# Performance work log

Hardware: AMD Instinct MI355X
Metric: run time of the kernel (lower is better)

## Reference

```python
import jax, jax.numpy as jnp
import numpy as np

N_NODES = 100000
NEG_SLOPE = 0.2  # PyG GATConv default leaky_relu slope


def _gat_conv(x, src, dst, W, a_src, a_dst, b, heads, out_c, concat):
    """One PyG-style GATConv (eval mode, dropout disabled).
    x: [N, F_in]; src/dst: [E] (src -> dst message direction, self-loops included).
    """
    N = x.shape[0]
    h = (x @ W).reshape(N, heads, out_c)                      # [N, H, C]
    alpha_s = jnp.einsum('nhc,hc->nh', h, a_src)              # [N, H]
    alpha_d = jnp.einsum('nhc,hc->nh', h, a_dst)              # [N, H]
    e = jax.nn.leaky_relu(alpha_s[src] + alpha_d[dst], NEG_SLOPE)  # [E, H]
    # segment softmax over incoming edges of each destination node
    e_max = jax.ops.segment_max(e, dst, num_segments=N)       # [N, H]
    e_exp = jnp.exp(e - e_max[dst])                           # [E, H]
    denom = jax.ops.segment_sum(e_exp, dst, num_segments=N)   # [N, H]
    alpha = e_exp / (denom[dst] + 1e-16)                      # [E, H]
    msg = h[src] * alpha[:, :, None]                          # [E, H, C]
    out = jax.ops.segment_sum(msg, dst, num_segments=N)       # [N, H, C]
    out = out.reshape(N, heads * out_c) if concat else out.mean(axis=1)
    return out + b


def setup_inputs() -> dict:
    key = jax.random.key(0)
    ks = jax.random.split(key, 16)
    N, E, F_in = N_NODES, 400000, 128
    H = 4
    h1, h2, out_dim = 128, 64, 2

    def glorot(k, shape, fan_in):
        return jax.random.normal(k, shape, dtype=jnp.float32) * (1.0 / np.sqrt(fan_in))

    inp = {
        'x': jax.random.normal(ks[0], (N, F_in), dtype=jnp.float32),
        'edge_index': jax.random.randint(ks[1], (2, E), 0, N, dtype=jnp.int64),
        'W1': glorot(ks[2], (F_in, H * h1), F_in),
        'a_src1': glorot(ks[3], (H, h1), h1),
        'a_dst1': glorot(ks[4], (H, h1), h1),
        'b1': jnp.zeros((H * h1,), dtype=jnp.float32),
        'W2': glorot(ks[5], (H * h1, H * h2), H * h1),
        'a_src2': glorot(ks[6], (H, h2), h2),
        'a_dst2': glorot(ks[7], (H, h2), h2),
        'b2': jnp.zeros((H * h2,), dtype=jnp.float32),
        # layer 3: 256 -> 2, heads=1, concat=False (mean)
        'W3': glorot(ks[8], (H * h2, 1 * out_dim), H * h2),
        'a_src3': glorot(ks[9], (1, out_dim), out_dim),
        'a_dst3': glorot(ks[10], (1, out_dim), out_dim),
        'b3': jnp.zeros((out_dim,), dtype=jnp.float32),
    }
    return inp


def reference(x, edge_index, W1, a_src1, a_dst1, b1, W2, a_src2, a_dst2, b2,
              W3, a_src3, a_dst3, b3):
    N = x.shape[0]
    # add self-loops (PyG GATConv default add_self_loops=True)
    loop = jnp.arange(N, dtype=edge_index.dtype)
    src = jnp.concatenate([edge_index[0], loop])
    dst = jnp.concatenate([edge_index[1], loop])

    h = _gat_conv(x, src, dst, W1, a_src1, a_dst1, b1, heads=4, out_c=128, concat=True)
    h = jax.nn.elu(h)  # dropout is identity in eval mode
    h = _gat_conv(h, src, dst, W2, a_src2, a_dst2, b2, heads=4, out_c=64, concat=True)
    h = jax.nn.elu(h)
    out = _gat_conv(h, src, dst, W3, a_src3, a_dst3, b3, heads=1, out_c=2, concat=False)
    return out
```

## Files before the change

### kernel.cpp

```cpp
#include <hip/hip_runtime.h>
#include <hip/hip_bf16.h>
#include <math.h>


#define LEAKY_SLOPE 0.2f

typedef __attribute__((ext_vector_type(8))) short bf16x8;
typedef __attribute__((ext_vector_type(4))) float f32x4;
typedef __attribute__((ext_vector_type(4))) float fx4;

__device__ __forceinline__ unsigned short f2bf(float f) {
    unsigned int x = __float_as_uint(f);
    x += 0x7fffu + ((x >> 16) & 1u);
    return (unsigned short)(x >> 16);
}
__device__ __forceinline__ float bf2f(unsigned short u) {
    return __uint_as_float(((unsigned int)u) << 16);
}
__device__ __forceinline__ float elu(float x) {
    return (x > 0.f) ? x : (__expf(x) - 1.f);
}

__device__ __forceinline__ void gll16(const void* g, void* l) {
    __builtin_amdgcn_global_load_lds((const __attribute__((address_space(1))) void*)g,
                                     (__attribute__((address_space(3))) void*)l, 16, 0, 0);
}

__device__ __forceinline__ int edge_val(const int* __restrict__ ei, int is64, long long idx) {
    return is64 ? ei[2 * idx] : ei[idx];
}

__global__ void detect_kernel(const unsigned int* __restrict__ ei, int* __restrict__ flag) {
    int lane = threadIdx.x;
    unsigned int v = ei[2 * lane + 1];
    unsigned long long b = __ballot(v != 0u);
    if (lane == 0) *flag = (b == 0ull) ? 1 : 0;
}

__global__ __launch_bounds__(256) void zero2_kernel(int* __restrict__ a, int* __restrict__ b, int n) {
    int i = blockIdx.x * blockDim.x + threadIdx.x;
    if (i < n) { a[i] = 0; b[i] = 0; }
}

__global__ __launch_bounds__(256) void sentinel_kernel(float* __restrict__ out, int n, float v) {
    int i = blockIdx.x * blockDim.x + threadIdx.x;
    if (i < n) out[i] = v;
}

__global__ __launch_bounds__(256) void count_kernel(const int* __restrict__ ei,
                                                    const int* __restrict__ flag,
                                                    int E, int N, int* __restrict__ counts) {
    int e = blockIdx.x * blockDim.x + threadIdx.x;
    if (e >= E + N) return;
    int is64 = *flag;
    int d = (e < E) ? edge_val(ei, is64, (long long)E + e) : (e - E);
    atomicAdd(&counts[d], 1);
}

__global__ __launch_bounds__(256) void scan_block_kernel(const int* __restrict__ counts,
                                                         int* __restrict__ ptrArr,
                                                         int* __restrict__ bsums, int N) {
    __shared__ int sh[256];
    int t = threadIdx.x, i = blockIdx.x * 256 + t;
    int v = (i < N) ? counts[i] : 0;
    sh[t] = v;
    __syncthreads();
    for (int off = 1; off < 256; off <<= 1) {
        int u = (t >= off) ? sh[t - off] : 0;
        __syncthreads();
        sh[t] += u;
        __syncthreads();
    }
    if (i < N) ptrArr[i] = sh[t] - v;
    if (t == 255) bsums[blockIdx.x] = sh[255];
}

__global__ __launch_bounds__(1024) void scan_tops_kernel(const int* __restrict__ bsums,
                                                         int* __restrict__ boff, int nb,
                                                         int* __restrict__ totalOut) {
    __shared__ int sh[1024];
    int t = threadIdx.x;
    int v = (t < nb) ? bsums[t] : 0;
    sh[t] = v;
    __syncthreads();
    for (int off = 1; off < 1024; off <<= 1) {
        int u = (t >= off) ? sh[t - off] : 0;
        __syncthreads();
        sh[t] += u;
        __syncthreads();
    }
    if (t < nb) boff[t] = sh[t] - v;
    if (t == 1023) *totalOut = sh[1023];
}

__global__ __launch_bounds__(256) void scan_add_kernel(int* __restrict__ ptrArr,
                                                       const int* __restrict__ boff, int N) {
    int i = blockIdx.x * blockDim.x + threadIdx.x;
    if (i < N) ptrArr[i] += boff[i >> 8];
}

__global__ __launch_bounds__(256) void fill_kernel(const int* __restrict__ ei,
                                                   const int* __restrict__ flag,
                                                   int E, int N,
                                                   const int* __restrict__ ptrArr,
                                                   int* __restrict__ cursor,
                                                   int* __restrict__ csr_src) {
    int e = blockIdx.x * blockDim.x + threadIdx.x;
    if (e >= E + N) return;
    int is64 = *flag;
    int s, d;
    if (e < E) {
        s = edge_val(ei, is64, e);
        d = edge_val(ei, is64, (long long)E + e);
    } else {
        s = d = e - E;
    }
    int slot = atomicAdd(&cursor[d], 1);
    csr_src[ptrArr[d] + slot] = s;
}

__global__ __launch_bounds__(256) void transpose_w_kernel(const float* __restrict__ W,
                                                          unsigned short* __restrict__ Wt,
                                                          int K, int Nn) {
    int i = blockIdx.x * blockDim.x + threadIdx.x;
    if (i >= K * Nn) return;
    int n = i / K, k = i - n * K;
    Wt[i] = f2bf(W[(size_t)k * Nn + n]);
}

__global__ __launch_bounds__(256) void proj_attn_kernel(const float* __restrict__ W1,
                                                        const float* __restrict__ a_s,
                                                        const float* __restrict__ a_d,
                                                        float* __restrict__ ws1,
                                                        float* __restrict__ wd1) {
    int t = blockIdx.x * blockDim.x + threadIdx.x;
    if (t >= 1024) return;
    int k = t >> 3, sd = (t >> 2) & 1, h = t & 3;
    const float* a = sd ? a_d : a_s;
    float s = 0.f;
    const float* wr = W1 + (size_t)k * 512 + h * 128;
    const float* ar = a + h * 128;
    for (int c = 0; c < 128; ++c) s += wr[c] * ar[c];
    (sd ? wd1 : ws1)[k * 4 + h] = s;
}

__global__ __launch_bounds__(256) void alpha_x_kernel(const float* __restrict__ x,
                                                      const float* __restrict__ ws1,
                                                      const float* __restrict__ wd1,
                                                      float* __restrict__ out_s,
                                                      float* __restrict__ out_d,
                                                      unsigned short* __restrict__ xbf, int N) {
    int lane = threadIdx.x & 63;
    int wid = threadIdx.x >> 6;
    int n = blockIdx.x * (blockDim.x >> 6) + wid;
    if (n >= N) return;
    int k0 = lane * 2;
    float2 xv = *(const float2*)(x + (size_t)n * 128 + k0);
    alignas(4) unsigned short o[2] = {f2bf(xv.x), f2bf(xv.y)};
    *(unsigned int*)(xbf + (size_t)n * 128 + k0) = *(unsigned int*)o;
    fx4 s0 = *(const fx4*)(ws1 + k0 * 4);
    fx4 s1 = *(const fx4*)(ws1 + k0 * 4 + 4);
    fx4 d0 = *(const fx4*)(wd1 + k0 * 4);
    fx4 d1 = *(const fx4*)(wd1 + k0 * 4 + 4);
    float ps[4], pd[4];
#pragma unroll
    for (int h = 0; h < 4; ++h) {
        ps[h] = xv.x * s0[h] + xv.y * s1[h];
        pd[h] = xv.x * d0[h] + xv.y * d1[h];
    }
#pragma unroll
    for (int off = 32; off; off >>= 1)
#pragma unroll
        for (int h = 0; h < 4; ++h) {
            ps[h] += __shfl_xor(ps[h], off);
            pd[h] += __shfl_xor(pd[h], off);
        }
    if (lane == 0) {
        fx4 rs = {ps[0], ps[1], ps[2], ps[3]};
        fx4 rd = {pd[0], pd[1], pd[2], pd[3]};
        *(fx4*)(out_s + (size_t)n * 4) = rs;
        *(fx4*)(out_d + (size_t)n * 4) = rd;
    }
}

__global__ __launch_bounds__(256) void sm_aggx_kernel(const int* __restrict__ ptrArr,
                                                      const int* __restrict__ csr_src,
                                                      const float* __restrict__ as,
                                                      const float* __restrict__ ad,
                                                      const unsigned short* __restrict__ xbf,
                                                      unsigned short* __restrict__ aggX, int N) {
    __shared__ float sal[4][64][4];
    int lane = threadIdx.x & 63;
    int wid = threadIdx.x >> 6;
    int n = blockIdx.x * 4 + wid;
    if (n >= N) return;
    int beg = ptrArr[n], end = ptrArr[n + 1];
    int deg = end - beg;
    fx4 dv = *(const fx4*)(ad + (size_t)n * 4);
    float acc[4][2];
#pragma unroll
    for (int h = 0; h < 4; ++h) { acc[h][0] = 0.f; acc[h][1] = 0.f; }

    if (deg <= 64) {
        bool act = lane < deg;
        int i = beg + (act ? lane : 0);
        int s = csr_src[i];
        fx4 av = *(const fx4*)(as + (size_t)s * 4);
        float e[4];
#pragma unroll
        for (int h = 0; h < 4; ++h) {
            float xx = av[h] + dv[h];
            xx = (xx >= 0.f) ? xx : LEAKY_SLOPE * xx;
            e[h] = act ? xx : -INFINITY;
        }
#pragma unroll
        for (int h = 0; h < 4; ++h) {
            float mm = e[h];
#pragma unroll
            for (int off = 32; off; off >>= 1) mm = fmaxf(mm, __shfl_xor(mm, off));
            float ex = __expf(e[h] - mm);
            float ss = ex;
#pragma unroll
            for (int off = 32; off; off >>= 1) ss += __shfl_xor(ss, off);
            sal[wid][lane][h] = ex / (ss + 1e-16f);
        }
        for (int i2 = beg; i2 < end; i2 += 4) {
            int r = end - i2;
            int e1 = (r > 1) ? i2 + 1 : i2;
            int e2 = (r > 2) ? i2 + 2 : i2;
            int e3 = (r > 3) ? i2 + 3 : i2;
            int s0 = csr_src[i2], s1 = csr_src[e1], s2 = csr_src[e2], s3 = csr_src[e3];
            fx4 a0 = *(const fx4*)&sal[wid][i2 - beg][0];
            fx4 a1 = *(const fx4*)&sal[wid][e1 - beg][0];
            fx4 a2 = *(const fx4*)&sal[wid][e2 - beg][0];
            fx4 a3 = *(const fx4*)&sal[wid][e3 - beg][0];
            if (r <= 1) a1 = (fx4){0.f, 0.f, 0.f, 0.f};
            if (r <= 2) a2 = (fx4){0.f, 0.f, 0.f, 0.f};
            if (r <= 3) a3 = (fx4){0.f, 0.f, 0.f, 0.f};
            unsigned int r0 = *(const unsigned int*)(xbf + (size_t)s0 * 128 + lane * 2);
            unsigned int r1 = *(const unsigned int*)(xbf + (size_t)s1 * 128 + lane * 2);
            unsigned int r2 = *(const unsigned int*)(xbf + (size_t)s2 * 128 + lane * 2);
            unsigned int r3 = *(const unsigned int*)(xbf + (size_t)s3 * 128 + lane * 2);
            float x00 = bf2f((unsigned short)r0), x01 = bf2f((unsigned short)(r0 >> 16));
            float x10 = bf2f((unsigned short)r1), x11 = bf2f((unsigned short)(r1 >> 16));
            float x20 = bf2f((unsigned short)r2), x21 = bf2f((unsigned short)(r2 >> 16));
            float x30 = bf2f((unsigned short)r3), x31 = bf2f((unsigned short)(r3 >> 16));
#pragma unroll
            for (int h = 0; h < 4; ++h) {
                acc[h][0] += a0[h] * x00 + a1[h] * x10 + a2[h] * x20 + a3[h] * x30;
                acc[h][1] += a0[h] * x01 + a1[h] * x11 + a2[h] * x21 + a3[h] * x31;
            }
        }
    } else {
        float m[4], inv[4];
#pragma unroll
        for (int h = 0; h < 4; ++h) m[h] = -INFINITY;
        for (int i = beg + lane; i < end; i += 64) {
            int s = csr_src[i];
            fx4 av = *(const fx4*)(as + (size_t)s * 4);
#pragma unroll
            for (int h = 0; h < 4; ++h) {
                float v = av[h] + dv[h];
                v = (v >= 0.f) ? v : LEAKY_SLOPE * v;
                m[h] = fmaxf(m[h], v);
            }
        }
#pragma unroll
        for (int h = 0; h < 4; ++h)
#pragma unroll
            for (int off = 32; off; off >>= 1) m[h] = fmaxf(m[h], __shfl_xor(m[h], off));
        float ss[4] = {0.f, 0.f, 0.f, 0.f};
        for (int i = beg + lane; i < end; i += 64) {
            int s = csr_src[i];
            fx4 av = *(const fx4*)(as + (size_t)s * 4);
#pragma unroll
            for (int h = 0; h < 4; ++h) {
                float v = av[h] + dv[h];
                v = (v >= 0.f) ? v : LEAKY_SLOPE * v;
                ss[h] += __expf(v - m[h]);
            }
        }
#pragma unroll
        for (int h = 0; h < 4; ++h) {
#pragma unroll
            for (int off = 32; off; off >>= 1) ss[h] += __shfl_xor(ss[h], off);
            inv[h] = 1.f / (ss[h] + 1e-16f);
        }
        for (int i = beg; i < end; ++i) {
            int s = csr_src[i];
            fx4 av = *(const fx4*)(as + (size_t)s * 4);
            unsigned int rr = *(const unsigned int*)(xbf + (size_t)s * 128 + lane * 2);
            float x0 = bf2f((unsigned short)rr), x1 = bf2f((unsigned short)(rr >> 16));
#pragma unroll
            for (int h = 0; h < 4; ++h) {
                float v = av[h] + dv[h];
                v = (v >= 0.f) ? v : LEAKY_SLOPE * v;
                float al = __expf(v - m[h]) * inv[h];
                acc[h][0] += al * x0;
                acc[h][1] += al * x1;
            }
        }
    }
#pragma unroll
    for (int h = 0; h < 4; ++h) {
        alignas(4) unsigned short o[2] = {f2bf(acc[h][0]), f2bf(acc[h][1])};
        *(unsigned int*)(aggX + (size_t)h * N * 128 + (size_t)n * 128 + lane * 2) = *(unsigned int*)o;
    }
}

__global__ __launch_bounds__(256) void fused12_kernel(const unsigned short* __restrict__ aggX,
                                                      const unsigned short* __restrict__ Wt1,
                                                      const unsigned short* __restrict__ Wt2,
                                                      const float* __restrict__ b1,
                                                      const float* __restrict__ a_src2,
                                                      const float* __restrict__ a_dst2,
                                                      unsigned short* __restrict__ h2,
                                                      float* __restrict__ alpha_s,
                                                      float* __restrict__ alpha_d,
                                                      int M) {
    __shared__ unsigned short h1[64 * 512];
    __shared__ unsigned short stg[4 * 64 * 128];
    const int bm = blockIdx.x;
    const int tid = threadIdx.x;
    const int lane = tid & 63, wid = tid >> 6;
    const int l15 = lane & 15, l4 = lane >> 4;

    const unsigned short* plane = aggX + (size_t)wid * M * 128;
    {
        char* base = (char*)stg + wid * 16384;
#pragma unroll
        for (int it = 0; it < 16; ++it) {
            int idx = it * 64 + lane;
            int row = idx >> 4, ch = idx & 15;
            int src = ch ^ (row & 7);
            int grow = bm * 64 + row;
            if (grow < M) gll16(plane + (size_t)grow * 128 + src * 8, base + it * 1024);
        }
    }
    __syncthreads();

    const char* Asw = (const char*)stg + wid * 16384;
    f32x4 acc[4][4];

    for (int half = 0; half < 2; ++half) {
#pragma unroll
        for (int m = 0; m < 4; ++m)
#pragma unroll
            for (int n = 0; n < 4; ++n) acc[m][n] = (f32x4){0.f, 0.f, 0.f, 0.f};
#pragma unroll
        for (int step = 0; step < 4; ++step) {
            bf16x8 af[4], bfr[4];
            int kb = step * 64 + l4 * 16;
#pragma unroll
            for (int m = 0; m < 4; ++m) {
                int rl = m * 16 + l15;
                af[m] = *(const bf16x8*)(Asw + rl * 256 + (kb ^ ((rl & 7) << 4)));
            }
#pragma unroll
            for (int n = 0; n < 4; ++n) {
                int rB = wid * 128 + half * 64 + n * 16 + l15;
                bfr[n] = *(const bf16x8*)(Wt1 + (size_t)rB * 128 + step * 32 + l4 * 8);
            }
#pragma unroll
            for (int m = 0; m < 4; ++m)
#pragma unroll
                for (int n = 0; n < 4; ++n)
                    acc[m][n] = __builtin_amdgcn_mfma_f32_16x16x32_bf16(bfr[n], af[m], acc[m][n], 0, 0, 0);
        }
#pragma unroll
        for (int m = 0; m < 4; ++m) {
            int rl = m * 16 + l15;
#pragma unroll
            for (int n = 0; n < 4; ++n) {
                int col = wid * 128 + half * 64 + n * 16 + l4 * 4;
                fx4 bb = *(const fx4*)(b1 + col);
                f32x4 v = acc[m][n];
                alignas(8) unsigned short o[4];
#pragma unroll
                for (int j = 0; j < 4; ++j) o[j] = f2bf(elu(v[j] + bb[j]));
                int byteoff = (col * 2) ^ ((rl & 7) << 4);
                *(uint2*)((char*)h1 + rl * 1024 + byteoff) = *(uint2*)o;
            }
        }
    }
    __syncthreads();

#pragma unroll
    for (int m = 0; m < 4; ++m)
#pragma unroll
        for (int n = 0; n < 4; ++n) acc[m][n] = (f32x4){0.f, 0.f, 0.f, 0.f};
    for (int step = 0; step < 16; ++step) {
        bf16x8 af[4], bfr[4];
        int kb = step * 64 + l4 * 16;
#pragma unroll
        for (int m = 0; m < 4; ++m) {
            int rl = m * 16 + l15;
            af[m] = *(const bf16x8*)((const char*)h1 + rl * 1024 + (kb ^ ((rl & 7) << 4)));
        }
#pragma unroll
        for (int n = 0; n < 4; ++n) {
            int rB = wid * 64 + n * 16 + l15;
            bfr[n] = *(const bf16x8*)(Wt2 + (size_t)rB * 512 + step * 32 + l4 * 8);
        }
#pragma unroll
        for (int m = 0; m < 4; ++m)
#pragma unroll
            for (int n = 0; n < 4; ++n)
                acc[m][n] = __builtin_amdgcn_mfma_f32_16x16x32_bf16(bfr[n], af[m], acc[m][n], 0, 0, 0);
    }
#pragma unroll
    for (int m = 0; m < 4; ++m) {
        int row = bm * 64 + m * 16 + l15;
        if (row < M) {
#pragma unroll
            for (int n = 0; n < 4; ++n) {
                int col = wid * 64 + n * 16 + l4 * 4;
                f32x4 v = acc[m][n];
                alignas(8) unsigned short o[4] = {f2bf(v[0]), f2bf(v[1]), f2bf(v[2]), f2bf(v[3])};
                *(uint2*)(h2 + (size_t)row * 256 + col) = *(uint2*)o;
            }
        }
    }
    float ps[4], pd[4];
#pragma unroll
    for (int m = 0; m < 4; ++m) { ps[m] = 0.f; pd[m] = 0.f; }
#pragma unroll
    for (int n = 0; n < 4; ++n) {
        int col = wid * 64 + n * 16 + l4 * 4;
        fx4 asv = *(const fx4*)(a_src2 + col);
        fx4 adv = *(const fx4*)(a_dst2 + col);
#pragma unroll
        for (int m = 0; m < 4; ++m)
#pragma unroll
            for (int j = 0; j < 4; ++j) {
                ps[m] += acc[m][n][j] * asv[j];
                pd[m] += acc[m][n][j] * adv[j];
            }
    }
#pragma unroll
    for (int m = 0; m < 4; ++m) {
        ps[m] += __shfl_xor(ps[m], 16); ps[m] += __shfl_xor(ps[m], 32);
        pd[m] += __shfl_xor(pd[m], 16); pd[m] += __shfl_xor(pd[m], 32);
    }
    if (lane < 16) {
#pragma unroll
        for (int m = 0; m < 4; ++m) {
            int row = bm * 64 + m * 16 + l15;
            if (row < M) {
                alpha_s[(size_t)row * 4 + wid] = ps[m];
                alpha_d[(size_t)row * 4 + wid] = pd[m];
            }
        }
    }
}

__global__ __launch_bounds__(256) void sm_agg2_kernel(const int* __restrict__ ptrArr,
                                                      const int* __restrict__ csr_src,
                                                      const float* __restrict__ as,
                                                      const float* __restrict__ ad,
                                                      const unsigned short* __restrict__ hmat,
                                                      const float* __restrict__ bias,
                                                      unsigned short* __restrict__ out, int N) {
    __shared__ float sal[4][64][4];
    int lane = threadIdx.x & 63;
    int wid = threadIdx.x >> 6;
    int n = blockIdx.x * 4 + wid;
    if (n >= N) return;
    int beg = ptrArr[n], end = ptrArr[n + 1];
    int deg = end - beg;
    int head = lane >> 4;
    fx4 dv = *(const fx4*)(ad + (size_t)n * 4);
    float acc[4] = {0.f, 0.f, 0.f, 0.f};

    if (deg <= 64) {
        bool act = lane < deg;
        int i = beg + (act ? lane : 0);
        int s = csr_src[i];
        fx4 av = *(const fx4*)(as + (size_t)s * 4);
        float e[4];
#pragma unroll
        for (int h = 0; h < 4; ++h) {
            float xx = av[h] + dv[h];
            xx = (xx >= 0.f) ? xx : LEAKY_SLOPE * xx;
            e[h] = act ? xx : -INFINITY;
        }
#pragma unroll
        for (int h = 0; h < 4; ++h) {
            float mm = e[h];
#pragma unroll
            for (int off = 32; off; off >>= 1) mm = fmaxf(mm, __shfl_xor(mm, off));
            float ex = __expf(e[h] - mm);
            float ss = ex;
#pragma unroll
            for (int off = 32; off; off >>= 1) ss += __shfl_xor(ss, off);
            sal[wid][lane][h] = ex / (ss + 1e-16f);
        }
        for (int i2 = beg; i2 < end; i2 += 4) {
            int r = end - i2;
            int e1 = (r > 1) ? i2 + 1 : i2;
            int e2 = (r > 2) ? i2 + 2 : i2;
            int e3 = (r > 3) ? i2 + 3 : i2;
            int s0 = csr_src[i2], s1 = csr_src[e1], s2 = csr_src[e2], s3 = csr_src[e3];
            float al0 = sal[wid][i2 - beg][head];
            float al1 = (r > 1) ? sal[wid][e1 - beg][head] : 0.f;
            float al2 = (r > 2) ? sal[wid][e2 - beg][head] : 0.f;
            float al3 = (r > 3) ? sal[wid][e3 - beg][head] : 0.f;
            alignas(8) unsigned short v0[4], v1[4], v2[4], v3[4];
            *(uint2*)v0 = *(const uint2*)(hmat + (size_t)s0 * 256 + lane * 4);
            *(uint2*)v1 = *(const uint2*)(hmat + (size_t)s1 * 256 + lane * 4);
            *(uint2*)v2 = *(const uint2*)(hmat + (size_t)s2 * 256 + lane * 4);
            *(uint2*)v3 = *(const uint2*)(hmat + (size_t)s3 * 256 + lane * 4);
#pragma unroll
            for (int t = 0; t < 4; ++t)
                acc[t] += al0 * bf2f(v0[t]) + al1 * bf2f(v1[t]) + al2 * bf2f(v2[t]) + al3 * bf2f(v3[t]);
        }
    } else {
        float m[4], inv[4];
#pragma unroll
        for (int h = 0; h < 4; ++h) m[h] = -INFINITY;
        for (int i = beg + lane; i < end; i += 64) {
            int s = csr_src[i];
            fx4 av = *(const fx4*)(as + (size_t)s * 4);
#pragma unroll
            for (int h = 0; h < 4; ++h) {
                float v = av[h] + dv[h];
                v = (v >= 0.f) ? v : LEAKY_SLOPE * v;
                m[h] = fmaxf(m[h], v);
            }
        }
#pragma unroll
        for (int h = 0; h < 4; ++h)
#pragma unroll
            for (int off = 32; off; off >>= 1) m[h] = fmaxf(m[h], __shfl_xor(m[h], off));
        float ss[4] = {0.f, 0.f, 0.f, 0.f};
        for (int i = beg + lane; i < end; i += 64) {
            int s = csr_src[i];
            fx4 av = *(const fx4*)(as + (size_t)s * 4);
#pragma unroll
            for (int h = 0; h < 4; ++h) {
                float v = av[h] + dv[h];
                v = (v >= 0.f) ? v : LEAKY_SLOPE * v;
                ss[h] += __expf(v - m[h]);
            }
        }
#pragma unroll
        for (int h = 0; h < 4; ++h) {
#pragma unroll
            for (int off = 32; off; off >>= 1) ss[h] += __shfl_xor(ss[h], off);
            inv[h] = 1.f / (ss[h] + 1e-16f);
        }
        float mh = m[head], invh = inv[head];
        float adh = dv[head];
        for (int i = beg; i < end; ++i) {
            int s = csr_src[i];
            float v = as[(size_t)s * 4 + head] + adh;
            v = (v >= 0.f) ? v : LEAKY_SLOPE * v;
            float al = __expf(v - mh) * invh;
            alignas(8) unsigned short vv[4];
            *(uint2*)vv = *(const uint2*)(hmat + (size_t)s * 256 + lane * 4);
#pragma unroll
            for (int t = 0; t < 4; ++t) acc[t] += al * bf2f(vv[t]);
        }
    }
    alignas(8) unsigned short o[4];
#pragma unroll
    for (int t = 0; t < 4; ++t) o[t] = f2bf(elu(acc[t] + bias[lane * 4 + t]));
    *(uint2*)(out + (size_t)n * 256 + lane * 4) = *(uint2*)o;
}

__global__ __launch_bounds__(256) void layer3_gemm_kernel(const unsigned short* __restrict__ x,
                                                          const float* __restrict__ W,
                                                          const float* __restrict__ a_s,
                                                          const float* __restrict__ a_d,
                                                          float* __restrict__ h3,
                                                          float* __restrict__ out_s,
                                                          float* __restrict__ out_d, int N) {
    int lane = threadIdx.x & 63;
    int wid = threadIdx.x >> 6;
    int n = blockIdx.x * (blockDim.x >> 6) + wid;
    if (n >= N) return;
    const unsigned short* xr = x + (size_t)n * 256 + lane * 4;
    alignas(8) unsigned short v[4];
    *(uint2*)v = *(const uint2*)xr;
    int k0 = lane * 4;
    fx4 w0 = *(const fx4*)(W + k0 * 2);
    fx4 w1 = *(const fx4*)(W + k0 * 2 + 4);
    float a0 = bf2f(v[0]) * w0[0] + bf2f(v[1]) * w0[2] + bf2f(v[2]) * w1[0] + bf2f(v[3]) * w1[2];
    float a1 = bf2f(v[0]) * w0[1] + bf2f(v[1]) * w0[3] + bf2f(v[2]) * w1[1] + bf2f(v[3]) * w1[3];
#pragma unroll
    for (int off = 32; off; off >>= 1) {
        a0 += __shfl_xor(a0, off);
        a1 += __shfl_xor(a1, off);
    }
    if (lane == 0) {
        h3[(size_t)n * 2 + 0] = a0;
        h3[(size_t)n * 2 + 1] = a1;
        out_s[n] = a0 * a_s[0] + a1 * a_s[1];
        out_d[n] = a0 * a_d[0] + a1 * a_d[1];
    }
}

__global__ __launch_bounds__(256) void sm_agg3_kernel(const int* __restrict__ ptrArr,
                                                      const int* __restrict__ csr_src,
                                                      const float* __restrict__ as,
                                                      const float* __restrict__ ad,
                                                      const float* __restrict__ h3,
                                                      const float* __restrict__ b3,
                                                      float* __restrict__ out, int N) {
    int lane = threadIdx.x & 63;
    int wid = threadIdx.x >> 6;
    int n = blockIdx.x * 4 + wid;
    if (n >= N) return;
    int beg = ptrArr[n], end = ptrArr[n + 1];
    int deg = end - beg;
    float adv = ad[n];
    float p0 = 0.f, p1 = 0.f;
    if (deg <= 64) {
        bool act = lane < deg;
        int i = beg + (act ? lane : 0);
        int s = csr_src[i];
        float xx = as[s] + adv;
        xx = (xx >= 0.f) ? xx : LEAKY_SLOPE * xx;
        float e = act ? xx : -INFINITY;
        float mm = e;
#pragma unroll
        for (int off = 32; off; off >>= 1) mm = fmaxf(mm, __shfl_xor(mm, off));
        float ex = __expf(e - mm);
        float ss = ex;
#pragma unroll
        for (int off = 32; off; off >>= 1) ss += __shfl_xor(ss, off);
        float al = ex / (ss + 1e-16f);
        float2 hv = act ? *(const float2*)(h3 + (size_t)s * 2) : make_float2(0.f, 0.f);
        p0 = al * hv.x;
        p1 = al * hv.y;
#pragma unroll
        for (int off = 32; off; off >>= 1) {
            p0 += __shfl_xor(p0, off);
            p1 += __shfl_xor(p1, off);
        }
    } else {
        float m = -INFINITY;
        for (int i = beg + lane; i < end; i += 64) {
            int s = csr_src[i];
            float v = as[s] + adv;
            v = (v >= 0.f) ? v : LEAKY_SLOPE * v;
            m = fmaxf(m, v);
        }
#pragma unroll
        for (int off = 32; off; off >>= 1) m = fmaxf(m, __shfl_xor(m, off));
        float ss = 0.f;
        for (int i = beg + lane; i < end; i += 64) {
            int s = csr_src[i];
            float v = as[s] + adv;
            v = (v >= 0.f) ? v : LEAKY_SLOPE * v;
            ss += __expf(v - m);
        }
#pragma unroll
        for (int off = 32; off; off >>= 1) ss += __shfl_xor(ss, off);
        float inv = 1.f / (ss + 1e-16f);
        for (int i = beg + lane; i < end; i += 64) {
            int s = csr_src[i];
            float v = as[s] + adv;
            v = (v >= 0.f) ? v : LEAKY_SLOPE * v;
            float al = __expf(v - m) * inv;
            float2 hv = *(const float2*)(h3 + (size_t)s * 2);
            p0 += al * hv.x;
            p1 += al * hv.y;
        }
#pragma unroll
        for (int off = 32; off; off >>= 1) {
            p0 += __shfl_xor(p0, off);
            p1 += __shfl_xor(p1, off);
        }
    }
    if (lane == 0) {
        out[(size_t)n * 2 + 0] = p0 + b3[0];
        out[(size_t)n * 2 + 1] = p1 + b3[1];
    }
}


extern "C" void kernel_launch(void* const* d_in, const int* in_sizes, int n_in,
                              void* d_out, int out_size, void* d_ws, size_t ws_size,
                              hipStream_t stream) {
    const float* x      = (const float*)d_in[0];
    const int*   ei     = (const int*)d_in[1];
    const float* W1     = (const float*)d_in[2];
    const float* a_src1 = (const float*)d_in[3];
    const float* a_dst1 = (const float*)d_in[4];
    const float* b1     = (const float*)d_in[5];
    const float* W2     = (const float*)d_in[6];
    const float* a_src2 = (const float*)d_in[7];
    const float* a_dst2 = (const float*)d_in[8];
    const float* b2     = (const float*)d_in[9];
    const float* W3     = (const float*)d_in[10];
    const float* a_src3 = (const float*)d_in[11];
    const float* a_dst3 = (const float*)d_in[12];
    const float* b3     = (const float*)d_in[13];

    const int N = in_sizes[0] / 128;
    const int E = in_sizes[1] / 2;
    const int ET = E + N;
    const int nb = (N + 255) / 256;

    size_t need = 0;
    auto carve = [&](size_t bytes) -> size_t {
        size_t off = need;
        need += (bytes + 255) & ~(size_t)255;
        return off;
    };
    size_t o_counts   = carve((size_t)N * 4);
    size_t o_cursor   = carve((size_t)N * 4);
    size_t o_ptr      = carve((size_t)(N + 1) * 4);
    size_t o_csr      = carve((size_t)ET * 4);
    size_t o_flag     = carve(4);
    size_t o_bsums    = carve((size_t)2048 * 4);
    size_t o_boff     = carve((size_t)2048 * 4);
    size_t o_alpha_s  = carve((size_t)N * 4 * 4);
    size_t o_alpha_d  = carve((size_t)N * 4 * 4);
    size_t o_h3       = carve((size_t)N * 2 * 4);
    size_t o_wsd      = carve((size_t)128 * 4 * 4 * 2);
    size_t o_wt1      = carve((size_t)512 * 128 * 2);
    size_t o_wt2      = carve((size_t)256 * 512 * 2);
    size_t o_xbf      = carve((size_t)N * 128 * 2);
    size_t o_bufA     = carve((size_t)N * 512 * 2);
    size_t o_bufB     = carve((size_t)N * 512 * 2);

    if (need > ws_size) {
        sentinel_kernel<<<(out_size + 255) / 256, 256, 0, stream>>>(
            (float*)d_out, out_size, (float)(ws_size >> 20));
        return;
    }

    char* w = (char*)d_ws;
    int*   counts   = (int*)(w + o_counts);
    int*   cursor   = (int*)(w + o_cursor);
    int*   ptrArr   = (int*)(w + o_ptr);
    int*   csr_src  = (int*)(w + o_csr);
    int*   flag     = (int*)(w + o_flag);
    int*   bsums    = (int*)(w + o_bsums);
    int*   boff     = (int*)(w + o_boff);
    float* alpha_s  = (float*)(w + o_alpha_s);
    float* alpha_d  = (float*)(w + o_alpha_d);
    float* h3       = (float*)(w + o_h3);
    float* ws1      = (float*)(w + o_wsd);
    float* wd1      = ws1 + 128 * 4;
    unsigned short* Wt1  = (unsigned short*)(w + o_wt1);
    unsigned short* Wt2  = (unsigned short*)(w + o_wt2);
    unsigned short* xbf  = (unsigned short*)(w + o_xbf);
    unsigned short* bufA = (unsigned short*)(w + o_bufA);
    unsigned short* bufB = (unsigned short*)(w + o_bufB);

    const int edge_blocks = (ET + 255) / 256;
    const int node_wave_blocks = (N + 3) / 4;
    const int node_thr_blocks = (N + 255) / 256;

    zero2_kernel<<<node_thr_blocks, 256, 0, stream>>>(counts, cursor, N);
    detect_kernel<<<1, 64, 0, stream>>>((const unsigned int*)ei, flag);
    count_kernel<<<edge_blocks, 256, 0, stream>>>(ei, flag, E, N, counts);
    scan_block_kernel<<<nb, 256, 0, stream>>>(counts, ptrArr, bsums, N);
    scan_tops_kernel<<<1, 1024, 0, stream>>>(bsums, boff, nb, ptrArr + N);
    scan_add_kernel<<<node_thr_blocks, 256, 0, stream>>>(ptrArr, boff, N);
    fill_kernel<<<edge_blocks, 256, 0, stream>>>(ei, flag, E, N, ptrArr, cursor, csr_src);

    transpose_w_kernel<<<(512 * 128 + 255) / 256, 256, 0, stream>>>(W1, Wt1, 128, 512);
    transpose_w_kernel<<<(256 * 512 + 255) / 256, 256, 0, stream>>>(W2, Wt2, 512, 256);
    proj_attn_kernel<<<4, 256, 0, stream>>>(W1, a_src1, a_dst1, ws1, wd1);

    alpha_x_kernel<<<node_wave_blocks, 256, 0, stream>>>(x, ws1, wd1, alpha_s, alpha_d, xbf, N);
    sm_aggx_kernel<<<node_wave_blocks, 256, 0, stream>>>(ptrArr, csr_src, alpha_s, alpha_d, xbf, bufA, N);

    fused12_kernel<<<(N + 63) / 64, 256, 0, stream>>>(bufA, Wt1, Wt2, b1,
                                                      a_src2, a_dst2, bufB,
                                                      alpha_s, alpha_d, N);

    sm_agg2_kernel<<<node_wave_blocks, 256, 0, stream>>>(ptrArr, csr_src, alpha_s, alpha_d, bufB, b2, bufA, N);

    layer3_gemm_kernel<<<node_wave_blocks, 256, 0, stream>>>(bufA, W3, a_src3, a_dst3, h3, alpha_s, alpha_d, N);
    sm_agg3_kernel<<<node_wave_blocks, 256, 0, stream>>>(ptrArr, csr_src, alpha_s, alpha_d, h3, b3, (float*)d_out, N);
}
```

Measured before the change: 442.0 us.

## Split fused layer-1/2 GEMM work across 8 waves per block

Doubles the fused12 block from 4 to 8 waves. Each wave now handles one head and one half of the output columns, in both the layer-1 GEMM and the layer-2 GEMM. The per-wave attention-logit partial sums are combined through shared memory with an extra barrier. The aim is more latency hiding and shorter per-wave serial MFMA chains, since the kernel uses about 96KB of LDS per block and occupancy is limited. The cost is an extra sync and reduction, plus redundant A-fragment loads from LDS across the wave pairs.

```diff
diff --git a/kernel.cpp b/kernel.cpp
--- a/kernel.cpp
+++ b/kernel.cpp
@@ -308,7 +308,7 @@
     }
 }
 
-__global__ __launch_bounds__(256) void fused12_kernel(const unsigned short* __restrict__ aggX,
+__global__ __launch_bounds__(512) void fused12_kernel(const unsigned short* __restrict__ aggX,
                                                       const unsigned short* __restrict__ Wt1,
                                                       const unsigned short* __restrict__ Wt2,
                                                       const float* __restrict__ b1,
@@ -323,26 +323,28 @@
     const int bm = blockIdx.x;
     const int tid = threadIdx.x;
     const int lane = tid & 63, wid = tid >> 6;
+    const int h = wid >> 1, half = wid & 1;
     const int l15 = lane & 15, l4 = lane >> 4;
 
-    const unsigned short* plane = aggX + (size_t)wid * M * 128;
+    const unsigned short* plane = aggX + (size_t)h * M * 128;
     {
-        char* base = (char*)stg + wid * 16384;
-#pragma unroll
-        for (int it = 0; it < 16; ++it) {
-            int idx = it * 64 + lane;
+        char* base = (char*)stg + h * 16384;
+#pragma unroll
+        for (int it = 0; it < 8; ++it) {
+            int j = half * 8 + it;
+            int idx = j * 64 + lane;
             int row = idx >> 4, ch = idx & 15;
             int src = ch ^ (row & 7);
             int grow = bm * 64 + row;
-            if (grow < M) gll16(plane + (size_t)grow * 128 + src * 8, base + it * 1024);
+            if (grow < M) gll16(plane + (size_t)grow * 128 + src * 8, base + j * 1024);
         }
     }
     __syncthreads();
 
-    const char* Asw = (const char*)stg + wid * 16384;
-    f32x4 acc[4][4];
-
-    for (int half = 0; half < 2; ++half) {
+    const char* Asw = (const char*)stg + h * 16384;
+
+    {
+        f32x4 acc[4][4];
 #pragma unroll
         for (int m = 0; m < 4; ++m)
 #pragma unroll
@@ -358,7 +360,7 @@
             }
 #pragma unroll
             for (int n = 0; n < 4; ++n) {
-                int rB = wid * 128 + half * 64 + n * 16 + l15;
+                int rB = h * 128 + half * 64 + n * 16 + l15;
                 bfr[n] = *(const bf16x8*)(Wt1 + (size_t)rB * 128 + step * 32 + l4 * 8);
             }
 #pragma unroll
@@ -372,7 +374,7 @@
             int rl = m * 16 + l15;
 #pragma unroll
             for (int n = 0; n < 4; ++n) {
-                int col = wid * 128 + half * 64 + n * 16 + l4 * 4;
+                int col = h * 128 + half * 64 + n * 16 + l4 * 4;
                 fx4 bb = *(const fx4*)(b1 + col);
                 f32x4 v = acc[m][n];
                 alignas(8) unsigned short o[4];
@@ -385,12 +387,14 @@
     }
     __syncthreads();
 
+    f32x4 acc2[4][2];
 #pragma unroll
     for (int m = 0; m < 4; ++m)
 #pragma unroll
-        for (int n = 0; n < 4; ++n) acc[m][n] = (f32x4){0.f, 0.f, 0.f, 0.f};
+        for (int n = 0; n < 2; ++n) acc2[m][n] = (f32x4){0.f, 0.f, 0.f, 0.f};
+#pragma unroll 4
     for (int step = 0; step < 16; ++step) {
-        bf16x8 af[4], bfr[4];
+        bf16x8 af[4], bfr[2];
         int kb = step * 64 + l4 * 16;
 #pragma unroll
         for (int m = 0; m < 4; ++m) {
@@ -398,24 +402,24 @@
             af[m] = *(const bf16x8*)((const char*)h1 + rl * 1024 + (kb ^ ((rl & 7) << 4)));
         }
 #pragma unroll
-        for (int n = 0; n < 4; ++n) {
-            int rB = wid * 64 + n * 16 + l15;
+        for (int n = 0; n < 2; ++n) {
+            int rB = h * 64 + half * 32 + n * 16 + l15;
             bfr[n] = *(const bf16x8*)(Wt2 + (size_t)rB * 512 + step * 32 + l4 * 8);
         }
 #pragma unroll
         for (int m = 0; m < 4; ++m)
 #pragma unroll
-            for (int n = 0; n < 4; ++n)
-                acc[m][n] = __builtin_amdgcn_mfma_f32_16x16x32_bf16(bfr[n], af[m], acc[m][n], 0, 0, 0);
+            for (int n = 0; n < 2; ++n)
+                acc2[m][n] = __builtin_amdgcn_mfma_f32_16x16x32_bf16(bfr[n], af[m], acc2[m][n], 0, 0, 0);
     }
 #pragma unroll
     for (int m = 0; m < 4; ++m) {
         int row = bm * 64 + m * 16 + l15;
         if (row < M) {
 #pragma unroll
-            for (int n = 0; n < 4; ++n) {
-                int col = wid * 64 + n * 16 + l4 * 4;
-                f32x4 v = acc[m][n];
+            for (int n = 0; n < 2; ++n) {
+                int col = h * 64 + half * 32 + n * 16 + l4 * 4;
+                f32x4 v = acc2[m][n];
                 alignas(8) unsigned short o[4] = {f2bf(v[0]), f2bf(v[1]), f2bf(v[2]), f2bf(v[3])};
                 *(uint2*)(h2 + (size_t)row * 256 + col) = *(uint2*)o;
             }
@@ -425,16 +429,16 @@
 #pragma unroll
     for (int m = 0; m < 4; ++m) { ps[m] = 0.f; pd[m] = 0.f; }
 #pragma unroll
-    for (int n = 0; n < 4; ++n) {
-        int col = wid * 64 + n * 16 + l4 * 4;
+    for (int n = 0; n < 2; ++n) {
+        int col = h * 64 + half * 32 + n * 16 + l4 * 4;
         fx4 asv = *(const fx4*)(a_src2 + col);
         fx4 adv = *(const fx4*)(a_dst2 + col);
 #pragma unroll
         for (int m = 0; m < 4; ++m)
 #pragma unroll
             for (int j = 0; j < 4; ++j) {
-                ps[m] += acc[m][n][j] * asv[j];
-                pd[m] += acc[m][n][j] * adv[j];
+                ps[m] += acc2[m][n][j] * asv[j];
+                pd[m] += acc2[m][n][j] * adv[j];
             }
     }
 #pragma unroll
@@ -442,13 +446,24 @@
         ps[m] += __shfl_xor(ps[m], 16); ps[m] += __shfl_xor(ps[m], 32);
         pd[m] += __shfl_xor(pd[m], 16); pd[m] += __shfl_xor(pd[m], 32);
     }
+    float* red = (float*)stg;
     if (lane < 16) {
 #pragma unroll
         for (int m = 0; m < 4; ++m) {
-            int row = bm * 64 + m * 16 + l15;
+            int rl = m * 16 + l15;
+            red[(wid * 2 + 0) * 64 + rl] = ps[m];
+            red[(wid * 2 + 1) * 64 + rl] = pd[m];
+        }
+    }
+    __syncthreads();
+    if (half == 0 && lane < 16) {
+#pragma unroll
+        for (int m = 0; m < 4; ++m) {
+            int rl = m * 16 + l15;
+            int row = bm * 64 + rl;
             if (row < M) {
-                alpha_s[(size_t)row * 4 + wid] = ps[m];
-                alpha_d[(size_t)row * 4 + wid] = pd[m];
+                alpha_s[(size_t)row * 4 + h] = red[(wid * 2 + 0) * 64 + rl] + red[((wid + 1) * 2 + 0) * 64 + rl];
+                alpha_d[(size_t)row * 4 + h] = red[(wid * 2 + 1) * 64 + rl] + red[((wid + 1) * 2 + 1) * 64 + rl];
             }
         }
     }
@@ -770,7 +785,7 @@
     alpha_x_kernel<<<node_wave_blocks, 256, 0, stream>>>(x, ws1, wd1, alpha_s, alpha_d, xbf, N);
     sm_aggx_kernel<<<node_wave_blocks, 256, 0, stream>>>(ptrArr, csr_src, alpha_s, alpha_d, xbf, bufA, N);
 
-    fused12_kernel<<<(N + 63) / 64, 256, 0, stream>>>(bufA, Wt1, Wt2, b1,
+    fused12_kernel<<<(N + 63) / 64, 512, 0, stream>>>(bufA, Wt1, Wt2, b1,
                                                       a_src2, a_dst2, bufB,
                                                       alpha_s, alpha_d, N);
 
```

After: 429.5 us. -2.8%, faster.
